# Performance work log

Hardware: AMD Instinct MI355X
Metric: run time of the kernel (lower is better)

Reference implementation:

```python
import jax, jax.numpy as jnp
import numpy as np

BS, SEQ, DIM, DIM_MLP, E = 2, 2048, 1024, 4096, 8
STD = 0.02  # nn.init.normal_(weight, std=0.02)


def setup_inputs() -> dict:
    key = jax.random.key(0)
    k_x, k_idx, k_w1, k_w2 = jax.random.split(key, 4)
    x = jax.random.normal(k_x, (BS, SEQ, DIM), dtype=jnp.float32)
    expert_idx = jax.random.randint(k_idx, (BS, SEQ), 0, E, dtype=jnp.int32)
    W1 = jax.random.normal(k_w1, (E, DIM, DIM_MLP), dtype=jnp.float32) * STD
    b1 = jnp.zeros((E, DIM_MLP), dtype=jnp.float32)
    W2 = jax.random.normal(k_w2, (E, DIM_MLP, DIM), dtype=jnp.float32) * STD
    b2 = jnp.zeros((E, DIM), dtype=jnp.float32)
    return {"x": x, "expert_idx": expert_idx, "W1": W1, "b1": b1, "W2": W2, "b2": b2}


def reference(x, expert_idx, W1, b1, W2, b2):
    # Compute ALL experts on all tokens (faithful to the torch module).
    # h: [bs, seq, E, dim_mlp]
    h = jnp.einsum("bsd,edm->bsem", x, W1) + b1
    h = jax.nn.gelu(h, approximate=False)  # torch nn.GELU default = exact erf
    # feat: [bs, seq, E, dim]  (== torch.cat along feature dim, reshaped)
    feat = jnp.einsum("bsem,emd->bsed", h, W2) + b2
    # Per-token gather of the assigned expert's output (top-1 select).
    idx = expert_idx.astype(jnp.int32)[:, :, None, None]  # [bs, seq, 1, 1]
    out = jnp.take_along_axis(feat, idx, axis=2)[:, :, 0, :]  # [bs, seq, dim]
    return out
```

## Files before the change

### kernel.cpp

```cpp
#include <hip/hip_runtime.h>
#include <hip/hip_bf16.h>
#include <math.h>

#define TOK   4096
#define DIM   1024
#define DMLP  4096
#define NE    8
#define BM    128
#define BN    128
#define BN2   64
#define BK    128
#define PADMAX (TOK + NE * BM)
#define NTILES (PADMAX / BM)
#define MAXSUP 24

typedef __attribute__((ext_vector_type(8))) short  short8;
typedef __attribute__((ext_vector_type(4))) float  float4v;
typedef __attribute__((ext_vector_type(4))) unsigned short ushort4v;
typedef __attribute__((ext_vector_type(2))) unsigned long long ull2;

#define ASYNC16(gp, lp) __builtin_amdgcn_global_load_lds( \
    (const __attribute__((address_space(1))) unsigned int*)(gp), \
    (__attribute__((address_space(3))) unsigned int*)(lp), 16, 0, 0)

#define SWZ(R, C) (((C) & 8) | (((C) ^ (R)) & 7))
#define FRAG_OFF(R, C) ((((R) << 4) + SWZ(R, C)) << 3)

static __device__ __forceinline__ unsigned short f2bf(float f) {
  unsigned u = __float_as_uint(f);
  u += 0x7fffu + ((u >> 16) & 1u);
  return (unsigned short)(u >> 16);
}

static __device__ __forceinline__ float gelu_erf(float v) {
  const float x = fabsf(v) * 0.70710678118654752f;
  const float t = __builtin_amdgcn_rcpf(1.0f + 0.3275911f * x);
  const float poly = ((((1.061405429f * t - 1.453152027f) * t + 1.421413741f) * t
                       - 0.284496736f) * t + 0.254829592f) * t;
  const float erf_abs = 1.0f - poly * __expf(-x * x);
  return 0.5f * v * (1.0f + copysignf(erf_abs, v));
}

__global__ void group_kernel(const int* __restrict__ eidx,
                             int* __restrict__ perm,
                             int* __restrict__ tile_e,
                             int* __restrict__ supA,
                             int* __restrict__ supB,
                             int* __restrict__ supE) {
  __shared__ int cnt[NE], off[NE], len[NE], cur[NE];
  const int tid = threadIdx.x;
  if (tid < NE) cnt[tid] = 0;
  __syncthreads();
  for (int i = tid; i < TOK; i += 256) atomicAdd(&cnt[eidx[i]], 1);
  __syncthreads();
  if (tid == 0) {
    int o = 0;
    for (int e = 0; e < NE; e++) {
      off[e] = o;
      len[e] = ((cnt[e] + BM - 1) / BM) * BM;
      cur[e] = o;
      o += len[e];
    }
    int ns = 0;
    for (int e = 0; e < NE; e++) {
      const int nt = len[e] / BM;
      for (int p = 0; p < nt; p += 2) {
        const int pb = (p + 1 < nt) ? (p + 1) : p;
        supA[ns] = off[e] + p * BM;
        supB[ns] = off[e] + pb * BM;
        supE[ns] = e;
        ns++;
      }
    }
    for (; ns < MAXSUP; ns++) { supA[ns] = 0; supB[ns] = 0; supE[ns] = -1; }
  }
  __syncthreads();
  for (int s = tid; s < PADMAX; s += 256) perm[s] = -1;
  __syncthreads();
  for (int i = tid; i < TOK; i += 256) {
    const int e = eidx[i];
    const int p = atomicAdd(&cur[e], 1);
    perm[p] = i;
  }
  __syncthreads();
  for (int t = tid; t < NTILES; t += 256) {
    const int row = t * BM;
    int te = -1;
    for (int e = 0; e < NE; e++)
      if (row >= off[e] && row < off[e] + len[e]) te = e;
    tile_e[t] = te;
  }
}

static __device__ __forceinline__
void conv_body(const float* __restrict__ W, unsigned short* __restrict__ WT,
               int K, int N, int bx, int by, int e, int tid,
               unsigned short T[64][68]) {
  const int k0 = by * 64, n0 = bx * 64;
  const float* Win = W + (size_t)e * K * N;
  unsigned short* Wout = WT + (size_t)e * K * N;
  const int i4 = tid & 15;
  const int kq = (tid >> 4) * 4;
  float4v v[4];
#pragma unroll
  for (int j = 0; j < 4; j++)
    v[j] = *(const float4v*)(Win + (size_t)(k0 + kq + j) * N + n0 + i4 * 4);
#pragma unroll
  for (int q = 0; q < 4; q++) {
    ushort4v w;
#pragma unroll
    for (int j = 0; j < 4; j++) w[j] = f2bf(v[j][q]);
    *(ushort4v*)&T[i4 * 4 + q][kq] = w;
  }
  __syncthreads();
  const int g  = tid & 7;
  const int nb = tid >> 3;
#pragma unroll
  for (int r = 0; r < 2; r++) {
    const int n = nb + 32 * r;
    const unsigned long long v0 = *(const unsigned long long*)&T[n][g * 8];
    const unsigned long long v1 = *(const unsigned long long*)&T[n][g * 8 + 4];
    ull2 o; o[0] = v0; o[1] = v1;
    *(ull2*)&Wout[(size_t)(n0 + n) * K + k0 + g * 8] = o;
  }
}

__global__ __launch_bounds__(256)
void prep_kernel(const float* __restrict__ W1, unsigned short* __restrict__ W1T,
                 const float* __restrict__ W2, unsigned short* __restrict__ W2T,
                 const float* __restrict__ x, const int* __restrict__ perm,
                 unsigned short* __restrict__ xg) {
  __shared__ unsigned short T[64][68];
  const int bid = blockIdx.x;
  const int tid = threadIdx.x;
  if (bid < 8192) {
    conv_body(W1, W1T, DIM, DMLP, bid & 63, (bid >> 6) & 15, bid >> 10, tid, T);
  } else if (bid < 16384) {
    const int b = bid - 8192;
    conv_body(W2, W2T, DMLP, DIM, b & 15, (b >> 4) & 63, b >> 10, tid, T);
  } else {
    const int slot = bid - 16384;
    const int t    = perm[slot];
    ushort4v o = (ushort4v){0, 0, 0, 0};
    if (t >= 0) {
      const float4v v = *(const float4v*)(x + (size_t)t * DIM + tid * 4);
#pragma unroll
      for (int q = 0; q < 4; q++) o[q] = f2bf(v[q]);
    }
    *(ushort4v*)(xg + (size_t)slot * DIM + tid * 4) = o;
  }
}

__global__ __launch_bounds__(256)
void gemm1_kernel(const unsigned short* __restrict__ xg,
                  const unsigned short* __restrict__ W1T,
                  const float* __restrict__ b1, const int* __restrict__ tile_e,
                  unsigned short* __restrict__ h) {
  const int bt = blockIdx.y;
  const int te = tile_e[bt];
  if (te < 0) return;
  const int n0 = blockIdx.x * BN;
  const unsigned short* Asrc = xg + (size_t)bt * BM * DIM;
  const unsigned short* Bsrc = W1T + (size_t)te * DIM * DMLP + (size_t)n0 * DIM;
  const int tid = threadIdx.x;

  __shared__ __align__(16) unsigned short SMEM[2 * BM * BK];

  const int rr = tid >> 4, q = tid & 15;
  const int cs = SWZ(rr, q);
  const unsigned short* a0 = Asrc + (size_t)rr * DIM + cs * 8;
  const unsigned short* b0 = Bsrc + (size_t)rr * DIM + cs * 8;

  const int wid = tid >> 6, lane = tid & 63;
  const int wm = (wid >> 1) * 64, wn = (wid & 1) * 64;
  const int l15 = lane & 15, quad = lane >> 4;

  float4v acc[4][4];
#pragma unroll
  for (int i = 0; i < 4; i++)
#pragma unroll
    for (int j = 0; j < 4; j++) acc[i][j] = (float4v){0.f, 0.f, 0.f, 0.f};

  for (int k0 = 0; k0 < DIM; k0 += BK) {
#pragma unroll
    for (int t = 0; t < 8; t++)
      ASYNC16(a0 + (size_t)(16 * t) * DIM + k0, &SMEM[(t * 256 + tid) * 8]);
#pragma unroll
    for (int t = 0; t < 8; t++)
      ASYNC16(b0 + (size_t)(16 * t) * DIM + k0, &SMEM[BM * BK + (t * 256 + tid) * 8]);
    __syncthreads();

#pragma unroll
    for (int hh = 0; hh < 4; hh++) {
      short8 a[4], b[4];
      const int C = hh * 4 + quad;
#pragma unroll
      for (int i = 0; i < 4; i++)
        a[i] = *(const short8*)&SMEM[FRAG_OFF(wm + i * 16 + l15, C)];
#pragma unroll
      for (int j = 0; j < 4; j++)
        b[j] = *(const short8*)&SMEM[BM * BK + FRAG_OFF(wn + j * 16 + l15, C)];
#pragma unroll
      for (int i = 0; i < 4; i++)
#pragma unroll
        for (int j = 0; j < 4; j++)
          acc[i][j] = __builtin_amdgcn_mfma_f32_16x16x32_bf16(a[i], b[j], acc[i][j], 0, 0, 0);
    }
    __syncthreads();
  }

#pragma unroll
  for (int i = 0; i < 4; i++) {
#pragma unroll
    for (int j = 0; j < 4; j++) {
      const int colL = wn + j * 16 + l15;
      const float bias = b1[te * DMLP + n0 + colL];
#pragma unroll
      for (int r = 0; r < 4; r++) {
        const int rowL = wm + i * 16 + quad * 4 + r;
        SMEM[rowL * BN + colL] = f2bf(gelu_erf(acc[i][j][r] + bias));
      }
    }
  }
  __syncthreads();
  const int gg = tid & 15;
  const int rb = tid >> 4;
#pragma unroll
  for (int p = 0; p < 8; p++) {
    const int rowL = rb + p * 16;
    const ull2 v = *(const ull2*)&SMEM[rowL * BN + gg * 8];
    *(ull2*)&h[(size_t)(bt * BM + rowL) * DMLP + n0 + gg * 8] = v;
  }
}

__global__ __launch_bounds__(256)
void gemm2_kernel(const unsigned short* __restrict__ h,
                  const unsigned short* __restrict__ W2T,
                  const float* __restrict__ b2, const int* __restrict__ perm,
                  const int* __restrict__ supA, const int* __restrict__ supB,
                  const int* __restrict__ supE, float* __restrict__ out) {
  const int s  = blockIdx.y;
  const int te = supE[s];
  if (te < 0) return;
  const int rowA = supA[s], rowB = supB[s];
  const int n0 = blockIdx.x * BN2;
  const int tid = threadIdx.x;

  __shared__ __align__(16) unsigned short As[256 * BK];
  __shared__ __align__(16) unsigned short Bs[BN2 * BK];

  const int rr = tid >> 4, q = tid & 15;
  const int cs = SWZ(rr, q);
  const unsigned short* aA = h + (size_t)(rowA + rr) * DMLP + cs * 8;
  const unsigned short* aB = h + (size_t)(rowB + rr) * DMLP + cs * 8;
  const unsigned short* b0 = W2T + (size_t)te * DMLP * DIM
                           + (size_t)(n0 + rr) * DMLP + cs * 8;

  const int wid = tid >> 6, lane = tid & 63;
  const int wm = wid * 64;
  const int l15 = lane & 15, quad = lane >> 4;

  float4v acc[4][4];
#pragma unroll
  for (int i = 0; i < 4; i++)
#pragma unroll
    for (int j = 0; j < 4; j++) acc[i][j] = (float4v){0.f, 0.f, 0.f, 0.f};

  for (int k0 = 0; k0 < DMLP; k0 += BK) {
#pragma unroll
    for (int t = 0; t < 8; t++)
      ASYNC16(aA + (size_t)(16 * t) * DMLP + k0, &As[(t * 256 + tid) * 8]);
#pragma unroll
    for (int t = 0; t < 8; t++)
      ASYNC16(aB + (size_t)(16 * t) * DMLP + k0, &As[((t + 8) * 256 + tid) * 8]);
#pragma unroll
    for (int t = 0; t < 4; t++)
      ASYNC16(b0 + (size_t)(16 * t) * DMLP + k0, &Bs[(t * 256 + tid) * 8]);
    __syncthreads();

#pragma unroll
    for (int hh = 0; hh < 4; hh++) {
      short8 a[4], b[4];
      const int C = hh * 4 + quad;
#pragma unroll
      for (int i = 0; i < 4; i++)
        a[i] = *(const short8*)&As[FRAG_OFF(wm + i * 16 + l15, C)];
#pragma unroll
      for (int j = 0; j < 4; j++)
        b[j] = *(const short8*)&Bs[FRAG_OFF(j * 16 + l15, C)];
#pragma unroll
      for (int i = 0; i < 4; i++)
#pragma unroll
        for (int j = 0; j < 4; j++)
          acc[i][j] = __builtin_amdgcn_mfma_f32_16x16x32_bf16(a[i], b[j], acc[i][j], 0, 0, 0);
    }
    __syncthreads();
  }

  const int halfbase = (wm < 128) ? (rowA + wm) : (rowB + (wm - 128));
#pragma unroll
  for (int i = 0; i < 4; i++) {
#pragma unroll
    for (int j = 0; j < 4; j++) {
      const int col = n0 + j * 16 + l15;
      const float bias = b2[te * DIM + col];
#pragma unroll
      for (int r = 0; r < 4; r++) {
        const int slot = halfbase + i * 16 + quad * 4 + r;
        const int t    = perm[slot];
        if (t >= 0) out[(size_t)t * DIM + col] = acc[i][j][r] + bias;
      }
    }
  }
}

extern "C" void kernel_launch(void* const* d_in, const int* in_sizes, int n_in,
                              void* d_out, int out_size, void* d_ws, size_t ws_size,
                              hipStream_t stream) {
  const float* x    = (const float*)d_in[0];
  const int*   eidx = (const int*)d_in[1];
  const float* W1   = (const float*)d_in[2];
  const float* b1   = (const float*)d_in[3];
  const float* W2   = (const float*)d_in[4];
  const float* b2   = (const float*)d_in[5];
  float* out = (float*)d_out;

  char* ws = (char*)d_ws;
  int* perm   = (int*)ws;
  int* tile_e = (int*)(ws + PADMAX * sizeof(int));
  int* supA   = (int*)(ws + 20736);
  int* supB   = (int*)(ws + 20832);
  int* supE   = (int*)(ws + 20928);
  unsigned short* xg  = (unsigned short*)(ws + 32768);
  unsigned short* h   = (unsigned short*)(ws + 32768 + 10485760);
  unsigned short* W1T = (unsigned short*)(ws + 32768 + 10485760 + 41943040);
  unsigned short* W2T = (unsigned short*)((char*)W1T + 67108864);

  group_kernel<<<1, 256, 0, stream>>>(eidx, perm, tile_e, supA, supB, supE);
  prep_kernel<<<16384 + PADMAX, 256, 0, stream>>>(W1, W1T, W2, W2T, x, perm, xg);
  gemm1_kernel<<<dim3(DMLP / BN, NTILES), 256, 0, stream>>>(xg, W1T, b1, tile_e, h);
  gemm2_kernel<<<dim3(DIM / BN2, MAXSUP), 256, 0, stream>>>(h, W2T, b2, perm, supA, supB, supE, out);
}
```

Baseline: 475.0 us.

## Fuse fp32 weight conversion and transpose into GEMM B-tile loads

After: 486.6 us. +2.4%, slower.

```diff
diff --git a/kernel.cpp b/kernel.cpp
--- a/kernel.cpp
+++ b/kernel.cpp
@@ -32,6 +32,12 @@
   return (unsigned short)(u >> 16);
 }
 
+static __device__ __forceinline__ unsigned cvt_pk_bf16(float lo, float hi) {
+  unsigned r;
+  asm("v_cvt_pk_bf16_f32 %0, %1, %2" : "=v"(r) : "v"(lo), "v"(hi));
+  return r;
+}
+
 static __device__ __forceinline__ float gelu_erf(float v) {
   const float x = fabsf(v) * 0.70710678118654752f;
   const float t = __builtin_amdgcn_rcpf(1.0f + 0.3275911f * x);
@@ -92,68 +98,24 @@
   }
 }
 
-static __device__ __forceinline__
-void conv_body(const float* __restrict__ W, unsigned short* __restrict__ WT,
-               int K, int N, int bx, int by, int e, int tid,
-               unsigned short T[64][68]) {
-  const int k0 = by * 64, n0 = bx * 64;
-  const float* Win = W + (size_t)e * K * N;
-  unsigned short* Wout = WT + (size_t)e * K * N;
-  const int i4 = tid & 15;
-  const int kq = (tid >> 4) * 4;
-  float4v v[4];
-#pragma unroll
-  for (int j = 0; j < 4; j++)
-    v[j] = *(const float4v*)(Win + (size_t)(k0 + kq + j) * N + n0 + i4 * 4);
-#pragma unroll
-  for (int q = 0; q < 4; q++) {
-    ushort4v w;
-#pragma unroll
-    for (int j = 0; j < 4; j++) w[j] = f2bf(v[j][q]);
-    *(ushort4v*)&T[i4 * 4 + q][kq] = w;
-  }
-  __syncthreads();
-  const int g  = tid & 7;
-  const int nb = tid >> 3;
-#pragma unroll
-  for (int r = 0; r < 2; r++) {
-    const int n = nb + 32 * r;
-    const unsigned long long v0 = *(const unsigned long long*)&T[n][g * 8];
-    const unsigned long long v1 = *(const unsigned long long*)&T[n][g * 8 + 4];
-    ull2 o; o[0] = v0; o[1] = v1;
-    *(ull2*)&Wout[(size_t)(n0 + n) * K + k0 + g * 8] = o;
-  }
-}
-
 __global__ __launch_bounds__(256)
-void prep_kernel(const float* __restrict__ W1, unsigned short* __restrict__ W1T,
-                 const float* __restrict__ W2, unsigned short* __restrict__ W2T,
-                 const float* __restrict__ x, const int* __restrict__ perm,
-                 unsigned short* __restrict__ xg) {
-  __shared__ unsigned short T[64][68];
-  const int bid = blockIdx.x;
-  const int tid = threadIdx.x;
-  if (bid < 8192) {
-    conv_body(W1, W1T, DIM, DMLP, bid & 63, (bid >> 6) & 15, bid >> 10, tid, T);
-  } else if (bid < 16384) {
-    const int b = bid - 8192;
-    conv_body(W2, W2T, DMLP, DIM, b & 15, (b >> 4) & 63, b >> 10, tid, T);
-  } else {
-    const int slot = bid - 16384;
-    const int t    = perm[slot];
-    ushort4v o = (ushort4v){0, 0, 0, 0};
-    if (t >= 0) {
-      const float4v v = *(const float4v*)(x + (size_t)t * DIM + tid * 4);
-#pragma unroll
-      for (int q = 0; q < 4; q++) o[q] = f2bf(v[q]);
-    }
-    *(ushort4v*)(xg + (size_t)slot * DIM + tid * 4) = o;
-  }
+void xgather_kernel(const float* __restrict__ x, const int* __restrict__ perm,
+                    unsigned short* __restrict__ xg) {
+  const int slot = blockIdx.x;
+  const int t    = perm[slot];
+  const int tid  = threadIdx.x;
+  ushort4v o = (ushort4v){0, 0, 0, 0};
+  if (t >= 0) {
+    const float4v v = *(const float4v*)(x + (size_t)t * DIM + tid * 4);
+#pragma unroll
+    for (int q = 0; q < 4; q++) o[q] = f2bf(v[q]);
+  }
+  *(ushort4v*)(xg + (size_t)slot * DIM + tid * 4) = o;
 }
 
 __global__ __launch_bounds__(256)
 void gemm1_kernel(const unsigned short* __restrict__ xg,
-                  const unsigned short* __restrict__ W1T,
+                  const float* __restrict__ W1,
                   const float* __restrict__ b1, const int* __restrict__ tile_e,
                   unsigned short* __restrict__ h) {
   const int bt = blockIdx.y;
@@ -161,7 +123,7 @@
   if (te < 0) return;
   const int n0 = blockIdx.x * BN;
   const unsigned short* Asrc = xg + (size_t)bt * BM * DIM;
-  const unsigned short* Bsrc = W1T + (size_t)te * DIM * DMLP + (size_t)n0 * DIM;
+  const float* Bsrc = W1 + (size_t)te * DIM * DMLP + n0;
   const int tid = threadIdx.x;
 
   __shared__ __align__(16) unsigned short SMEM[2 * BM * BK];
@@ -169,7 +131,8 @@
   const int rr = tid >> 4, q = tid & 15;
   const int cs = SWZ(rr, q);
   const unsigned short* a0 = Asrc + (size_t)rr * DIM + cs * 8;
-  const unsigned short* b0 = Bsrc + (size_t)rr * DIM + cs * 8;
+
+  const int tk = tid & 7, t3 = tid >> 3;
 
   const int wid = tid >> 6, lane = tid & 63;
   const int wm = (wid >> 1) * 64, wn = (wid & 1) * 64;
@@ -183,11 +146,26 @@
 
   for (int k0 = 0; k0 < DIM; k0 += BK) {
 #pragma unroll
+    for (int p = 0; p < 4; p++) {
+      const int kt  = tk + p * 8;
+      const int k0t = kt * 4;
+      float4v v[4];
+#pragma unroll
+      for (int j = 0; j < 4; j++)
+        v[j] = *(const float4v*)(Bsrc + (size_t)(k0 + k0t + j) * DMLP + t3 * 4);
+      const int C = k0t >> 3, h2 = kt & 1;
+#pragma unroll
+      for (int qq = 0; qq < 4; qq++) {
+        const int n = t3 * 4 + qq;
+        const unsigned w0 = cvt_pk_bf16(v[0][qq], v[1][qq]);
+        const unsigned w1 = cvt_pk_bf16(v[2][qq], v[3][qq]);
+        *(unsigned long long*)&SMEM[BM * BK + FRAG_OFF(n, C) + h2 * 4] =
+            ((unsigned long long)w1 << 32) | w0;
+      }
+    }
+#pragma unroll
     for (int t = 0; t < 8; t++)
       ASYNC16(a0 + (size_t)(16 * t) * DIM + k0, &SMEM[(t * 256 + tid) * 8]);
-#pragma unroll
-    for (int t = 0; t < 8; t++)
-      ASYNC16(b0 + (size_t)(16 * t) * DIM + k0, &SMEM[BM * BK + (t * 256 + tid) * 8]);
     __syncthreads();
 
 #pragma unroll
@@ -235,7 +213,7 @@
 
 __global__ __launch_bounds__(256)
 void gemm2_kernel(const unsigned short* __restrict__ h,
-                  const unsigned short* __restrict__ W2T,
+                  const float* __restrict__ W2,
                   const float* __restrict__ b2, const int* __restrict__ perm,
                   const int* __restrict__ supA, const int* __restrict__ supB,
                   const int* __restrict__ supE, float* __restrict__ out) {
@@ -253,8 +231,11 @@
   const int cs = SWZ(rr, q);
   const unsigned short* aA = h + (size_t)(rowA + rr) * DMLP + cs * 8;
   const unsigned short* aB = h + (size_t)(rowB + rr) * DMLP + cs * 8;
-  const unsigned short* b0 = W2T + (size_t)te * DMLP * DIM
-                           + (size_t)(n0 + rr) * DMLP + cs * 8;
+  const float* Bsrc = W2 + (size_t)te * DMLP * DIM + n0;
+
+  const int tk = tid & 7, t3 = tid >> 3;
+  const int nt = t3 & 15;
+  const int kh = t3 >> 4;
 
   const int wid = tid >> 6, lane = tid & 63;
   const int wm = wid * 64;
@@ -268,14 +249,29 @@
 
   for (int k0 = 0; k0 < DMLP; k0 += BK) {
 #pragma unroll
+    for (int p = 0; p < 2; p++) {
+      const int kt  = tk + kh * 8 + p * 16;
+      const int k0t = kt * 4;
+      float4v v[4];
+#pragma unroll
+      for (int j = 0; j < 4; j++)
+        v[j] = *(const float4v*)(Bsrc + (size_t)(k0 + k0t + j) * DIM + nt * 4);
+      const int C = k0t >> 3, h2 = kt & 1;
+#pragma unroll
+      for (int qq = 0; qq < 4; qq++) {
+        const int n = nt * 4 + qq;
+        const unsigned w0 = cvt_pk_bf16(v[0][qq], v[1][qq]);
+        const unsigned w1 = cvt_pk_bf16(v[2][qq], v[3][qq]);
+        *(unsigned long long*)&Bs[FRAG_OFF(n, C) + h2 * 4] =
+            ((unsigned long long)w1 << 32) | w0;
+      }
+    }
+#pragma unroll
     for (int t = 0; t < 8; t++)
       ASYNC16(aA + (size_t)(16 * t) * DMLP + k0, &As[(t * 256 + tid) * 8]);
 #pragma unroll
     for (int t = 0; t < 8; t++)
       ASYNC16(aB + (size_t)(16 * t) * DMLP + k0, &As[((t + 8) * 256 + tid) * 8]);
-#pragma unroll
-    for (int t = 0; t < 4; t++)
-      ASYNC16(b0 + (size_t)(16 * t) * DMLP + k0, &Bs[(t * 256 + tid) * 8]);
     __syncthreads();
 
 #pragma unroll
@@ -333,11 +329,9 @@
   int* supE   = (int*)(ws + 20928);
   unsigned short* xg  = (unsigned short*)(ws + 32768);
   unsigned short* h   = (unsigned short*)(ws + 32768 + 10485760);
-  unsigned short* W1T = (unsigned short*)(ws + 32768 + 10485760 + 41943040);
-  unsigned short* W2T = (unsigned short*)((char*)W1T + 67108864);
 
   group_kernel<<<1, 256, 0, stream>>>(eidx, perm, tile_e, supA, supB, supE);
-  prep_kernel<<<16384 + PADMAX, 256, 0, stream>>>(W1, W1T, W2, W2T, x, perm, xg);
-  gemm1_kernel<<<dim3(DMLP / BN, NTILES), 256, 0, stream>>>(xg, W1T, b1, tile_e, h);
-  gemm2_kernel<<<dim3(DIM / BN2, MAXSUP), 256, 0, stream>>>(h, W2T, b2, perm, supA, supB, supE, out);
-}
+  xgather_kernel<<<PADMAX, 256, 0, stream>>>(x, perm, xg);
+  gemm1_kernel<<<dim3(DMLP / BN, NTILES), 256, 0, stream>>>(xg, W1, b1, tile_e, h);
+  gemm2_kernel<<<dim3(DIM / BN2, MAXSUP), 256, 0, stream>>>(h, W2, b2, perm, supA, supB, supE, out);
+}
```

## Pack weights into k-group-major bf16 layout, removing LDS transpose in prep

Applied to the files above, without the earlier changes.

Result: faster. 463.9 us (-2.3%).

```diff
diff --git a/kernel.cpp b/kernel.cpp
--- a/kernel.cpp
+++ b/kernel.cpp
@@ -25,6 +25,7 @@
 
 #define SWZ(R, C) (((C) & 8) | (((C) ^ (R)) & 7))
 #define FRAG_OFF(R, C) ((((R) << 4) + SWZ(R, C)) << 3)
+#define BOFF(C, n) ((((C) << 7) + (n)) << 3)
 
 static __device__ __forceinline__ unsigned short f2bf(float f) {
   unsigned u = __float_as_uint(f);
@@ -93,35 +94,20 @@
 }
 
 static __device__ __forceinline__
-void conv_body(const float* __restrict__ W, unsigned short* __restrict__ WT,
-               int K, int N, int bx, int by, int e, int tid,
-               unsigned short T[64][68]) {
-  const int k0 = by * 64, n0 = bx * 64;
-  const float* Win = W + (size_t)e * K * N;
-  unsigned short* Wout = WT + (size_t)e * K * N;
-  const int i4 = tid & 15;
-  const int kq = (tid >> 4) * 4;
-  float4v v[4];
-#pragma unroll
-  for (int j = 0; j < 4; j++)
-    v[j] = *(const float4v*)(Win + (size_t)(k0 + kq + j) * N + n0 + i4 * 4);
+void convpack_body(const float* __restrict__ W, unsigned short* __restrict__ WT,
+                   int K, int N, int kg, int nblk, int e, int tid) {
+  const int n0 = nblk * 1024 + tid * 4;
+  const float* Win = W + (size_t)e * K * N + (size_t)kg * 8 * N + n0;
+  unsigned short* Wout = WT + (size_t)e * K * N + ((size_t)kg * N + n0) * 8;
+  float4v v[8];
+#pragma unroll
+  for (int j = 0; j < 8; j++) v[j] = *(const float4v*)(Win + (size_t)j * N);
 #pragma unroll
   for (int q = 0; q < 4; q++) {
-    ushort4v w;
-#pragma unroll
-    for (int j = 0; j < 4; j++) w[j] = f2bf(v[j][q]);
-    *(ushort4v*)&T[i4 * 4 + q][kq] = w;
-  }
-  __syncthreads();
-  const int g  = tid & 7;
-  const int nb = tid >> 3;
-#pragma unroll
-  for (int r = 0; r < 2; r++) {
-    const int n = nb + 32 * r;
-    const unsigned long long v0 = *(const unsigned long long*)&T[n][g * 8];
-    const unsigned long long v1 = *(const unsigned long long*)&T[n][g * 8 + 4];
-    ull2 o; o[0] = v0; o[1] = v1;
-    *(ull2*)&Wout[(size_t)(n0 + n) * K + k0 + g * 8] = o;
+    short8 g;
+#pragma unroll
+    for (int j = 0; j < 8; j++) g[j] = (short)f2bf(v[j][q]);
+    *(short8*)(Wout + q * 8) = g;
   }
 }
 
@@ -130,16 +116,15 @@
                  const float* __restrict__ W2, unsigned short* __restrict__ W2T,
                  const float* __restrict__ x, const int* __restrict__ perm,
                  unsigned short* __restrict__ xg) {
-  __shared__ unsigned short T[64][68];
   const int bid = blockIdx.x;
   const int tid = threadIdx.x;
-  if (bid < 8192) {
-    conv_body(W1, W1T, DIM, DMLP, bid & 63, (bid >> 6) & 15, bid >> 10, tid, T);
-  } else if (bid < 16384) {
-    const int b = bid - 8192;
-    conv_body(W2, W2T, DMLP, DIM, b & 15, (b >> 4) & 63, b >> 10, tid, T);
+  if (bid < 4096) {
+    convpack_body(W1, W1T, DIM, DMLP, bid & 127, (bid >> 7) & 3, bid >> 9, tid);
+  } else if (bid < 8192) {
+    const int b = bid - 4096;
+    convpack_body(W2, W2T, DMLP, DIM, b & 511, 0, b >> 9, tid);
   } else {
-    const int slot = bid - 16384;
+    const int slot = bid - 8192;
     const int t    = perm[slot];
     ushort4v o = (ushort4v){0, 0, 0, 0};
     if (t >= 0) {
@@ -161,7 +146,7 @@
   if (te < 0) return;
   const int n0 = blockIdx.x * BN;
   const unsigned short* Asrc = xg + (size_t)bt * BM * DIM;
-  const unsigned short* Bsrc = W1T + (size_t)te * DIM * DMLP + (size_t)n0 * DIM;
+  const unsigned short* Bsrc = W1T + (size_t)te * DIM * DMLP + (size_t)n0 * 8;
   const int tid = threadIdx.x;
 
   __shared__ __align__(16) unsigned short SMEM[2 * BM * BK];
@@ -169,7 +154,8 @@
   const int rr = tid >> 4, q = tid & 15;
   const int cs = SWZ(rr, q);
   const unsigned short* a0 = Asrc + (size_t)rr * DIM + cs * 8;
-  const unsigned short* b0 = Bsrc + (size_t)rr * DIM + cs * 8;
+  const int bC = tid >> 7, bn = tid & 127;
+  const unsigned short* b0 = Bsrc + ((size_t)bC * DMLP + bn) * 8;
 
   const int wid = tid >> 6, lane = tid & 63;
   const int wm = (wid >> 1) * 64, wn = (wid & 1) * 64;
@@ -182,12 +168,14 @@
     for (int j = 0; j < 4; j++) acc[i][j] = (float4v){0.f, 0.f, 0.f, 0.f};
 
   for (int k0 = 0; k0 < DIM; k0 += BK) {
+    const int kg0 = k0 >> 3;
 #pragma unroll
     for (int t = 0; t < 8; t++)
       ASYNC16(a0 + (size_t)(16 * t) * DIM + k0, &SMEM[(t * 256 + tid) * 8]);
 #pragma unroll
     for (int t = 0; t < 8; t++)
-      ASYNC16(b0 + (size_t)(16 * t) * DIM + k0, &SMEM[BM * BK + (t * 256 + tid) * 8]);
+      ASYNC16(b0 + (size_t)(kg0 + 2 * t) * DMLP * 8,
+              &SMEM[BM * BK + (t * 256 + tid) * 8]);
     __syncthreads();
 
 #pragma unroll
@@ -199,7 +187,7 @@
         a[i] = *(const short8*)&SMEM[FRAG_OFF(wm + i * 16 + l15, C)];
 #pragma unroll
       for (int j = 0; j < 4; j++)
-        b[j] = *(const short8*)&SMEM[BM * BK + FRAG_OFF(wn + j * 16 + l15, C)];
+        b[j] = *(const short8*)&SMEM[BM * BK + BOFF(C, wn + j * 16 + l15)];
 #pragma unroll
       for (int i = 0; i < 4; i++)
 #pragma unroll
@@ -247,14 +235,15 @@
   const int tid = threadIdx.x;
 
   __shared__ __align__(16) unsigned short As[256 * BK];
-  __shared__ __align__(16) unsigned short Bs[BN2 * BK];
+  __shared__ __align__(16) unsigned short Bs[16 * BN2 * 8];
 
   const int rr = tid >> 4, q = tid & 15;
   const int cs = SWZ(rr, q);
   const unsigned short* aA = h + (size_t)(rowA + rr) * DMLP + cs * 8;
   const unsigned short* aB = h + (size_t)(rowB + rr) * DMLP + cs * 8;
+  const int bC = tid >> 6, bn = tid & 63;
   const unsigned short* b0 = W2T + (size_t)te * DMLP * DIM
-                           + (size_t)(n0 + rr) * DMLP + cs * 8;
+                           + ((size_t)bC * DIM + n0 + bn) * 8;
 
   const int wid = tid >> 6, lane = tid & 63;
   const int wm = wid * 64;
@@ -267,6 +256,7 @@
     for (int j = 0; j < 4; j++) acc[i][j] = (float4v){0.f, 0.f, 0.f, 0.f};
 
   for (int k0 = 0; k0 < DMLP; k0 += BK) {
+    const int kg0 = k0 >> 3;
 #pragma unroll
     for (int t = 0; t < 8; t++)
       ASYNC16(aA + (size_t)(16 * t) * DMLP + k0, &As[(t * 256 + tid) * 8]);
@@ -275,7 +265,7 @@
       ASYNC16(aB + (size_t)(16 * t) * DMLP + k0, &As[((t + 8) * 256 + tid) * 8]);
 #pragma unroll
     for (int t = 0; t < 4; t++)
-      ASYNC16(b0 + (size_t)(16 * t) * DMLP + k0, &Bs[(t * 256 + tid) * 8]);
+      ASYNC16(b0 + (size_t)(kg0 + 4 * t) * DIM * 8, &Bs[(t * 256 + tid) * 8]);
     __syncthreads();
 
 #pragma unroll
@@ -287,7 +277,7 @@
         a[i] = *(const short8*)&As[FRAG_OFF(wm + i * 16 + l15, C)];
 #pragma unroll
       for (int j = 0; j < 4; j++)
-        b[j] = *(const short8*)&Bs[FRAG_OFF(j * 16 + l15, C)];
+        b[j] = *(const short8*)&Bs[(((C) << 6) + j * 16 + l15) << 3];
 #pragma unroll
       for (int i = 0; i < 4; i++)
 #pragma unroll
@@ -337,7 +327,7 @@
   unsigned short* W2T = (unsigned short*)((char*)W1T + 67108864);
 
   group_kernel<<<1, 256, 0, stream>>>(eidx, perm, tile_e, supA, supB, supE);
-  prep_kernel<<<16384 + PADMAX, 256, 0, stream>>>(W1, W1T, W2, W2T, x, perm, xg);
+  prep_kernel<<<8192 + PADMAX, 256, 0, stream>>>(W1, W1T, W2, W2T, x, perm, xg);
   gemm1_kernel<<<dim3(DMLP / BN, NTILES), 256, 0, stream>>>(xg, W1T, b1, tile_e, h);
   gemm2_kernel<<<dim3(DIM / BN2, MAXSUP), 256, 0, stream>>>(h, W2T, b2, perm, supA, supB, supE, out);
 }
```
